# Performance work log

Hardware: AMD Instinct MI355X
Metric: run time of the kernel (lower is better)

Reference implementation:

```python
import jax, jax.numpy as jnp
import numpy as np

CE_W, DICE_W, BD_W = 1.0, 3.0, 2.0   # combined-loss lambdas
BPW = 10.0                            # boundary pixel weight
SMOOTH = 1e-6                         # dice smoothing
# cv2.getStructuringElement(cv2.MORPH_ELLIPSE, (5,5))
ELLIPSE5 = np.array([[0,0,1,0,0],
                     [1,1,1,1,1],
                     [1,1,1,1,1],
                     [1,1,1,1,1],
                     [0,0,1,0,0]], dtype=bool)


def setup_inputs() -> dict:
    key = jax.random.key(0)
    k1, k2 = jax.random.split(key)
    B, C, H, W = 8, 8, 512, 1024
    pred = jax.random.normal(k1, (B, C, H, W), dtype=jnp.float32)
    target = jax.random.randint(k2, (B, H, W), 0, C).astype(jnp.int32)
    return {"pred": pred, "target": target}


def _morph(mask, is_dilate):
    """Grayscale dilate/erode with 5x5 ellipse SE (matches cv2 default border:
    padding value never wins the max/min)."""
    pad_val = 0 if is_dilate else jnp.iinfo(jnp.int32).max
    p = jnp.pad(mask, ((0, 0), (2, 2), (2, 2)), constant_values=pad_val)
    H, W = mask.shape[1], mask.shape[2]
    out = None
    for dy in range(5):
        for dx in range(5):
            if not ELLIPSE5[dy, dx]:
                continue
            s = p[:, dy:dy + H, dx:dx + W]
            if out is None:
                out = s
            else:
                out = jnp.maximum(out, s) if is_dilate else jnp.minimum(out, s)
    return out


def reference(pred, target):
    B, C, H, W = pred.shape
    logp = jax.nn.log_softmax(pred, axis=1)                         # (B,C,H,W)
    # per-pixel cross entropy
    ce_map = -jnp.take_along_axis(logp, target[:, None], axis=1)[:, 0]  # (B,H,W)
    ce = ce_map.mean()
    # dice over softmax probs vs one-hot target
    probs = jnp.exp(logp)
    onehot = jax.nn.one_hot(target, C, dtype=pred.dtype, axis=1)    # (B,C,H,W)
    inter = jnp.sum(probs * onehot, axis=(2, 3))                    # (B,C)
    card = jnp.sum(probs, axis=(2, 3)) + jnp.sum(onehot, axis=(2, 3))
    dice = 1.0 - jnp.mean((2.0 * inter + SMOOTH) / (card + SMOOTH))
    # boundary mask = morphological gradient of the label map
    t = target.astype(jnp.int32)
    boundary = _morph(t, True) - _morph(t, False)                   # (B,H,W)
    wmap = jnp.where(boundary > 0, jnp.float32(BPW), jnp.float32(1.0))
    bd = jnp.mean(ce_map * wmap)
    return CE_W * ce + DICE_W * dice + BD_W * bd
```

## Files before the change

### kernel.cpp

```cpp
#include <hip/hip_runtime.h>
#include <math.h>

constexpr int B = 8, C = 8, H = 512, W = 1024;
constexpr int RH = 2;
constexpr int NT = 256;
constexpr float BPW = 10.0f;
constexpr float SMOOTH = 1e-6f;

constexpr int ACC_N = 2 * B + 3 * B * C;

constexpr int NVALS = 22;
constexpr int PSTRIDE = 24;

typedef float f32x4 __attribute__((ext_vector_type(4)));

__device__ __forceinline__ void gl_lds16(const float* g, float* l) {
    __builtin_amdgcn_global_load_lds(
        (const __attribute__((address_space(1))) void*)g,
        (__attribute__((address_space(3))) void*)l,
        16, 0, 0);
}

__device__ __forceinline__ unsigned win_or5(unsigned lo, unsigned mid, unsigned hi) {
    unsigned long long a = ((unsigned long long)mid << 32) | lo;
    unsigned long long b = ((unsigned long long)hi << 32) | mid;
    return (unsigned)(a >> 16) | (unsigned)(a >> 24) | mid |
           (unsigned)(b >> 8) | (unsigned)(b >> 16);
}

__device__ __forceinline__ unsigned pack_row(const int* __restrict__ tb, int gh, int gc) {
    if (gh < 0 || gh >= H || gc < 0 || gc >= W) return 0u;
    const int4 t4 = *reinterpret_cast<const int4*>(tb + (size_t)gh * W + gc);
    return (1u << t4.x) | ((1u << t4.y) << 8) | ((1u << t4.z) << 16) | ((1u << t4.w) << 24);
}

__global__ __launch_bounds__(NT)
void loss_main(const float* __restrict__ pred, const int* __restrict__ target,
               float* __restrict__ acc) {
    __shared__ float lds_pred[RH * C * W];
    __shared__ float sred[32 * PSTRIDE];

    const int tid = threadIdx.x;
    const int lane = tid & 63, wid = tid >> 6;
    const int h0 = blockIdx.x * RH;
    const int b  = blockIdx.y;
    const int gc = tid * 4;

    const int* tb = target + (size_t)b * H * W;
    const size_t plane = (size_t)H * W;

    const unsigned c0 = pack_row(tb, h0 - 2, gc);
    const unsigned c1 = pack_row(tb, h0 - 1, gc);
    const unsigned c2 = pack_row(tb, h0,     gc);
    const unsigned c3 = pack_row(tb, h0 + 1, gc);
    const unsigned c4 = pack_row(tb, h0 + 2, gc);
    const unsigned c5 = pack_row(tb, h0 + 3, gc);
    const unsigned l0 = pack_row(tb, h0 - 1, gc - 4);
    const unsigned l1 = pack_row(tb, h0,     gc - 4);
    const unsigned l2 = pack_row(tb, h0 + 1, gc - 4);
    const unsigned l3 = pack_row(tb, h0 + 2, gc - 4);
    const unsigned r0 = pack_row(tb, h0 - 1, gc + 4);
    const unsigned r1 = pack_row(tb, h0,     gc + 4);
    const unsigned r2 = pack_row(tb, h0 + 1, gc + 4);
    const unsigned r3 = pack_row(tb, h0 + 2, gc + 4);

    const int seg = wid * 256;
#pragma unroll
    for (int s = 0; s < RH; ++s)
#pragma unroll
        for (int c = 0; c < C; ++c) {
            const float* g = pred + ((size_t)(b * C + c)) * plane
                                  + (size_t)(h0 + s) * W + seg + lane * 4;
            float* l = &lds_pred[(s * C + c) * W + seg];
            gl_lds16(g, l);
        }

    const unsigned bmA = win_or5(l0 | l1 | l2, c1 | c2 | c3, r0 | r1 | r2) | c0 | c4;
    const unsigned bmB = win_or5(l1 | l2 | l3, c2 | c3 | c4, r1 | r2 | r3) | c1 | c5;

    __builtin_amdgcn_sched_barrier(0);
    asm volatile("s_waitcnt vmcnt(0)" ::: "memory");
    __builtin_amdgcn_sched_barrier(0);

    float ce_s = 0.f, bd_s = 0.f;
    float p_s[C], in_s[C];
    unsigned cnt = 0u;
#pragma unroll
    for (int c = 0; c < C; ++c) { p_s[c] = 0.f; in_s[c] = 0.f; }

#pragma unroll
    for (int s = 0; s < RH; ++s) {
        f32x4 x[C];
#pragma unroll
        for (int c = 0; c < C; ++c)
            x[c] = *reinterpret_cast<const f32x4*>(&lds_pred[(s * C + c) * W + gc]);

        const unsigned cmid = (s == 0) ? c2 : c3;
        const unsigned bm4  = (s == 0) ? bmA : bmB;

#pragma unroll
        for (int j = 0; j < 4; ++j) {
            const float x0 = (j==0)?x[0].x:(j==1)?x[0].y:(j==2)?x[0].z:x[0].w;
            const float x1 = (j==0)?x[1].x:(j==1)?x[1].y:(j==2)?x[1].z:x[1].w;
            const float x2 = (j==0)?x[2].x:(j==1)?x[2].y:(j==2)?x[2].z:x[2].w;
            const float x3 = (j==0)?x[3].x:(j==1)?x[3].y:(j==2)?x[3].z:x[3].w;
            const float x4 = (j==0)?x[4].x:(j==1)?x[4].y:(j==2)?x[4].z:x[4].w;
            const float x5 = (j==0)?x[5].x:(j==1)?x[5].y:(j==2)?x[5].z:x[5].w;
            const float x6 = (j==0)?x[6].x:(j==1)?x[6].y:(j==2)?x[6].z:x[6].w;
            const float x7 = (j==0)?x[7].x:(j==1)?x[7].y:(j==2)?x[7].z:x[7].w;

            const float e0 = __expf(x0), e1 = __expf(x1), e2 = __expf(x2), e3 = __expf(x3);
            const float e4 = __expf(x4), e5 = __expf(x5), e6 = __expf(x6), e7 = __expf(x7);
            const float sum = ((e0 + e1) + (e2 + e3)) + ((e4 + e5) + (e6 + e7));
            const float invs = __builtin_amdgcn_rcpf(sum);

            const unsigned cm  = (cmid >> (8 * j)) & 0xFFu;
            const unsigned bmj = (bm4  >> (8 * j)) & 0xFFu;
            const int t = 31 - __clz(cm);

            const float p0 = e0 * invs, p1 = e1 * invs, p2 = e2 * invs, p3 = e3 * invs;
            const float p4 = e4 * invs, p5 = e5 * invs, p6 = e6 * invs, p7 = e7 * invs;
            p_s[0] += p0; p_s[1] += p1; p_s[2] += p2; p_s[3] += p3;
            p_s[4] += p4; p_s[5] += p5; p_s[6] += p6; p_s[7] += p7;

            const bool b0 = (t == 0), b1 = (t == 1), b2 = (t == 2), b3 = (t == 3);
            const bool b4 = (t == 4), b5 = (t == 5), b6 = (t == 6), b7 = (t == 7);
            in_s[0] += b0 ? p0 : 0.f;  in_s[1] += b1 ? p1 : 0.f;
            in_s[2] += b2 ? p2 : 0.f;  in_s[3] += b3 ? p3 : 0.f;
            in_s[4] += b4 ? p4 : 0.f;  in_s[5] += b5 ? p5 : 0.f;
            in_s[6] += b6 ? p6 : 0.f;  in_s[7] += b7 ? p7 : 0.f;

            float pt = p0;
            pt = b1 ? p1 : pt;  pt = b2 ? p2 : pt;  pt = b3 ? p3 : pt;
            pt = b4 ? p4 : pt;  pt = b5 ? p5 : pt;  pt = b6 ? p6 : pt;
            pt = b7 ? p7 : pt;
            const float l = __logf(pt);
            const float wgt = (bmj & (bmj - 1u)) ? BPW : 1.f;
            ce_s -= l;
            bd_s = fmaf(-l, wgt, bd_s);
            cnt += 1u << (t << 2);
        }
    }

    float vals[NVALS];
    vals[0] = ce_s; vals[1] = bd_s;
#pragma unroll
    for (int c = 0; c < C; ++c) {
        vals[2 + c]  = p_s[c];
        vals[10 + c] = in_s[c];
    }
#pragma unroll
    for (int q = 0; q < 4; ++q) {
        const float lo = (float)((cnt >> (8 * q)) & 0xFu);
        const float hi = (float)((cnt >> (8 * q + 4)) & 0xFu);
        vals[18 + q] = lo + 4096.f * hi;
    }
#pragma unroll
    for (int k = 0; k < NVALS; ++k) {
        float v = vals[k];
        v += __shfl_down(v, 32, 64);
        v += __shfl_down(v, 16, 64);
        v += __shfl_down(v, 8, 64);
        vals[k] = v;
    }
    if (lane < 8) {
        const int p = wid * 8 + lane;
#pragma unroll
        for (int k = 0; k < NVALS; ++k) sred[p * PSTRIDE + k] = vals[k];
    }
    __syncthreads();

    const int k = tid >> 3, j = tid & 7;
    if (k < NVALS) {
        float v = sred[(0 * 8 + j) * PSTRIDE + k] + sred[(1 * 8 + j) * PSTRIDE + k]
                + sred[(2 * 8 + j) * PSTRIDE + k] + sred[(3 * 8 + j) * PSTRIDE + k];
        v += __shfl_down(v, 4, 64);
        v += __shfl_down(v, 2, 64);
        v += __shfl_down(v, 1, 64);
        if (j == 0) {
            if (k == 0)      atomicAdd(&acc[b], v);
            else if (k == 1) atomicAdd(&acc[B + b], v);
            else if (k < 10) atomicAdd(&acc[2 * B + b * C + (k - 2)], v);
            else if (k < 18) atomicAdd(&acc[2 * B + B * C + b * C + (k - 10)], v);
            else {
                const int q = k - 18;
                const float hi = floorf(v * (1.f / 4096.f));
                const float lo = v - 4096.f * hi;
                atomicAdd(&acc[2 * B + 2 * B * C + b * C + 2 * q],     lo);
                atomicAdd(&acc[2 * B + 2 * B * C + b * C + 2 * q + 1], hi);
            }
        }
    }
}

__global__ void loss_final(const float* __restrict__ acc, float* __restrict__ out) {
    const int i = threadIdx.x;
    const float psum  = acc[2 * B + i];
    const float inter = acc[2 * B + B * C + i];
    const float cnt   = acc[2 * B + 2 * B * C + i];
    float d = (2.f * inter + SMOOTH) / (psum + cnt + SMOOTH);
    float ce = (i < B) ? acc[i] : 0.f;
    float bd = (i < B) ? acc[B + i] : 0.f;
#pragma unroll
    for (int off = 32; off > 0; off >>= 1) d += __shfl_down(d, off, 64);
#pragma unroll
    for (int off = 4; off > 0; off >>= 1) {
        ce += __shfl_down(ce, off, 64);
        bd += __shfl_down(bd, off, 64);
    }
    if (i == 0) {
        const float N = (float)B * H * W;
        const float dice = 1.f - d / (float)(B * C);
        out[0] = 1.0f * (ce / N) + 3.0f * dice + 2.0f * (bd / N);
    }
}

extern "C" void kernel_launch(void* const* d_in, const int* in_sizes, int n_in,
                              void* d_out, int out_size, void* d_ws, size_t ws_size,
                              hipStream_t stream) {
    const float* pred = (const float*)d_in[0];
    const int* target = (const int*)d_in[1];
    float* acc = (float*)d_ws;
    float* out = (float*)d_out;

    hipMemsetAsync(acc, 0, ACC_N * sizeof(float), stream);

    dim3 grid(H / RH, B);
    loss_main<<<grid, NT, 0, stream>>>(pred, target, acc);
    loss_final<<<1, 64, 0, stream>>>(acc, out);
}
```

Measured before the change: 224.3 us.

## Process eight rows per block with double-buffered LDS prefetch and shared label halo

Each block now handles 8 rows instead of 2. It packs the label rows plus a halo into LDS once, so the boundary masks reuse neighbour data instead of re-reading target rows from global memory. Prediction rows are double-buffered in LDS with async global-to-LDS loads, so the next row's load overlaps compute on the current row. Per-class counts move to a 64-bit packed counter reduced as integers, which gives fewer atomics per pixel handled. In exchange the grid has four times fewer blocks and the LDS and register pressure is higher, which could lower occupancy.

```diff
diff --git a/kernel.cpp b/kernel.cpp
--- a/kernel.cpp
+++ b/kernel.cpp
@@ -2,7 +2,7 @@
 #include <math.h>
 
 constexpr int B = 8, C = 8, H = 512, W = 1024;
-constexpr int RH = 2;
+constexpr int ROWS = 8;
 constexpr int NT = 256;
 constexpr float BPW = 10.0f;
 constexpr float SMOOTH = 1e-6f;
@@ -10,7 +10,9 @@
 constexpr int ACC_N = 2 * B + 3 * B * C;
 
 constexpr int NVALS = 22;
-constexpr int PSTRIDE = 24;
+constexpr int PSTRIDE = 23;
+constexpr int TGROWS = ROWS + 4;
+constexpr int TSTRIDE = W / 4 + 2;
 
 typedef float f32x4 __attribute__((ext_vector_type(4)));
 
@@ -28,75 +30,102 @@
            (unsigned)(b >> 8) | (unsigned)(b >> 16);
 }
 
-__device__ __forceinline__ unsigned pack_row(const int* __restrict__ tb, int gh, int gc) {
-    if (gh < 0 || gh >= H || gc < 0 || gc >= W) return 0u;
-    const int4 t4 = *reinterpret_cast<const int4*>(tb + (size_t)gh * W + gc);
-    return (1u << t4.x) | ((1u << t4.y) << 8) | ((1u << t4.z) << 16) | ((1u << t4.w) << 24);
-}
-
 __global__ __launch_bounds__(NT)
 void loss_main(const float* __restrict__ pred, const int* __restrict__ target,
                float* __restrict__ acc) {
-    __shared__ float lds_pred[RH * C * W];
+    __shared__ float lds_pred[2 * C * W];
     __shared__ float sred[32 * PSTRIDE];
+    unsigned* tpk = reinterpret_cast<unsigned*>(&lds_pred[C * W]);
 
     const int tid = threadIdx.x;
     const int lane = tid & 63, wid = tid >> 6;
-    const int h0 = blockIdx.x * RH;
+    const int r0 = blockIdx.x * ROWS;
     const int b  = blockIdx.y;
     const int gc = tid * 4;
-
-    const int* tb = target + (size_t)b * H * W;
     const size_t plane = (size_t)H * W;
-
-    const unsigned c0 = pack_row(tb, h0 - 2, gc);
-    const unsigned c1 = pack_row(tb, h0 - 1, gc);
-    const unsigned c2 = pack_row(tb, h0,     gc);
-    const unsigned c3 = pack_row(tb, h0 + 1, gc);
-    const unsigned c4 = pack_row(tb, h0 + 2, gc);
-    const unsigned c5 = pack_row(tb, h0 + 3, gc);
-    const unsigned l0 = pack_row(tb, h0 - 1, gc - 4);
-    const unsigned l1 = pack_row(tb, h0,     gc - 4);
-    const unsigned l2 = pack_row(tb, h0 + 1, gc - 4);
-    const unsigned l3 = pack_row(tb, h0 + 2, gc - 4);
-    const unsigned r0 = pack_row(tb, h0 - 1, gc + 4);
-    const unsigned r1 = pack_row(tb, h0,     gc + 4);
-    const unsigned r2 = pack_row(tb, h0 + 1, gc + 4);
-    const unsigned r3 = pack_row(tb, h0 + 2, gc + 4);
-
+    const int* tb = target + (size_t)b * plane;
+    const float* pbase = pred + (size_t)b * C * plane;
     const int seg = wid * 256;
-#pragma unroll
-    for (int s = 0; s < RH; ++s)
-#pragma unroll
-        for (int c = 0; c < C; ++c) {
-            const float* g = pred + ((size_t)(b * C + c)) * plane
-                                  + (size_t)(h0 + s) * W + seg + lane * 4;
-            float* l = &lds_pred[(s * C + c) * W + seg];
-            gl_lds16(g, l);
-        }
-
-    const unsigned bmA = win_or5(l0 | l1 | l2, c1 | c2 | c3, r0 | r1 | r2) | c0 | c4;
-    const unsigned bmB = win_or5(l1 | l2 | l3, c2 | c3 | c4, r1 | r2 | r3) | c1 | c5;
-
+
+    int4 traw[TGROWS];
+#pragma unroll
+    for (int j = 0; j < TGROWS; ++j) {
+        int gh = r0 - 2 + j;
+        gh = gh < 0 ? 0 : (gh >= H ? H - 1 : gh);
+        traw[j] = *reinterpret_cast<const int4*>(tb + (size_t)gh * W + gc);
+    }
     __builtin_amdgcn_sched_barrier(0);
-    asm volatile("s_waitcnt vmcnt(0)" ::: "memory");
-    __builtin_amdgcn_sched_barrier(0);
+
+#pragma unroll
+    for (int c = 0; c < C; ++c)
+        gl_lds16(pbase + (size_t)c * plane + (size_t)r0 * W + seg + lane * 4,
+                 &lds_pred[c * W + seg]);
+
+#pragma unroll
+    for (int j = 0; j < TGROWS; ++j) {
+        const int gh = r0 - 2 + j;
+        const int4 t4 = traw[j];
+        const unsigned m = (1u << t4.x) | ((1u << t4.y) << 8) |
+                           ((1u << t4.z) << 16) | ((1u << t4.w) << 24);
+        tpk[j * TSTRIDE + 1 + tid] = (gh >= 0 && gh < H) ? m : 0u;
+    }
+    if (tid < 2 * TGROWS) {
+        const int j = tid >> 1;
+        tpk[j * TSTRIDE + ((tid & 1) ? (TSTRIDE - 1) : 0)] = 0u;
+    }
+    __syncthreads();
+
+    unsigned bm4s[ROWS], cmids[ROWS];
+    {
+        unsigned m[TGROWS], lf[TGROWS], rg[TGROWS];
+#pragma unroll
+        for (int j = 0; j < TGROWS; ++j) {
+            m[j]  = tpk[j * TSTRIDE + 1 + tid];
+            lf[j] = tpk[j * TSTRIDE + tid];
+            rg[j] = tpk[j * TSTRIDE + 2 + tid];
+        }
+#pragma unroll
+        for (int i = 0; i < ROWS; ++i) {
+            bm4s[i] = win_or5(lf[i+1] | lf[i+2] | lf[i+3],
+                              m[i+1]  | m[i+2]  | m[i+3],
+                              rg[i+1] | rg[i+2] | rg[i+3]) | m[i] | m[i+4];
+            cmids[i] = m[i + 2];
+        }
+    }
+    __syncthreads();
 
     float ce_s = 0.f, bd_s = 0.f;
     float p_s[C], in_s[C];
-    unsigned cnt = 0u;
+    unsigned long long cnt = 0ull;
 #pragma unroll
     for (int c = 0; c < C; ++c) { p_s[c] = 0.f; in_s[c] = 0.f; }
 
 #pragma unroll
-    for (int s = 0; s < RH; ++s) {
+    for (int i = 0; i < ROWS; ++i) {
+        const int cur = i & 1;
+        if (i < ROWS - 1) {
+            asm volatile("s_waitcnt lgkmcnt(0)" ::: "memory");
+            __builtin_amdgcn_sched_barrier(0);
+#pragma unroll
+            for (int c = 0; c < C; ++c)
+                gl_lds16(pbase + (size_t)c * plane + (size_t)(r0 + i + 1) * W + seg + lane * 4,
+                         &lds_pred[(cur ^ 1) * C * W + c * W + seg]);
+            __builtin_amdgcn_sched_barrier(0);
+            asm volatile("s_waitcnt vmcnt(8)" ::: "memory");
+            __builtin_amdgcn_sched_barrier(0);
+        } else {
+            __builtin_amdgcn_sched_barrier(0);
+            asm volatile("s_waitcnt vmcnt(0)" ::: "memory");
+            __builtin_amdgcn_sched_barrier(0);
+        }
+
+        const unsigned bm4  = bm4s[i];
+        const unsigned cmid = cmids[i];
+
         f32x4 x[C];
 #pragma unroll
         for (int c = 0; c < C; ++c)
-            x[c] = *reinterpret_cast<const f32x4*>(&lds_pred[(s * C + c) * W + gc]);
-
-        const unsigned cmid = (s == 0) ? c2 : c3;
-        const unsigned bm4  = (s == 0) ? bmA : bmB;
+            x[c] = *reinterpret_cast<const f32x4*>(&lds_pred[cur * C * W + c * W + gc]);
 
 #pragma unroll
         for (int j = 0; j < 4; ++j) {
@@ -138,11 +167,12 @@
             const float wgt = (bmj & (bmj - 1u)) ? BPW : 1.f;
             ce_s -= l;
             bd_s = fmaf(-l, wgt, bd_s);
-            cnt += 1u << (t << 2);
-        }
-    }
-
-    float vals[NVALS];
+            cnt += 1ull << (t << 3);
+        }
+    }
+
+    float vals[18];
+    unsigned uvals[4];
     vals[0] = ce_s; vals[1] = bd_s;
 #pragma unroll
     for (int c = 0; c < C; ++c) {
@@ -150,44 +180,60 @@
         vals[10 + c] = in_s[c];
     }
 #pragma unroll
-    for (int q = 0; q < 4; ++q) {
-        const float lo = (float)((cnt >> (8 * q)) & 0xFu);
-        const float hi = (float)((cnt >> (8 * q + 4)) & 0xFu);
-        vals[18 + q] = lo + 4096.f * hi;
-    }
-#pragma unroll
-    for (int k = 0; k < NVALS; ++k) {
+    for (int q = 0; q < 4; ++q)
+        uvals[q] = (unsigned)((cnt >> (16 * q)) & 0xFFull)
+                 | ((unsigned)((cnt >> (16 * q + 8)) & 0xFFull) << 16);
+
+#pragma unroll
+    for (int k = 0; k < 18; ++k) {
         float v = vals[k];
         v += __shfl_down(v, 32, 64);
         v += __shfl_down(v, 16, 64);
         v += __shfl_down(v, 8, 64);
         vals[k] = v;
     }
+#pragma unroll
+    for (int q = 0; q < 4; ++q) {
+        unsigned v = uvals[q];
+        v += (unsigned)__shfl_down((int)v, 32, 64);
+        v += (unsigned)__shfl_down((int)v, 16, 64);
+        v += (unsigned)__shfl_down((int)v, 8, 64);
+        uvals[q] = v;
+    }
+    unsigned* sredu = reinterpret_cast<unsigned*>(sred);
     if (lane < 8) {
         const int p = wid * 8 + lane;
 #pragma unroll
-        for (int k = 0; k < NVALS; ++k) sred[p * PSTRIDE + k] = vals[k];
+        for (int k = 0; k < 18; ++k) sred[p * PSTRIDE + k] = vals[k];
+#pragma unroll
+        for (int q = 0; q < 4; ++q) sredu[p * PSTRIDE + 18 + q] = uvals[q];
     }
     __syncthreads();
 
     const int k = tid >> 3, j = tid & 7;
     if (k < NVALS) {
-        float v = sred[(0 * 8 + j) * PSTRIDE + k] + sred[(1 * 8 + j) * PSTRIDE + k]
-                + sred[(2 * 8 + j) * PSTRIDE + k] + sred[(3 * 8 + j) * PSTRIDE + k];
-        v += __shfl_down(v, 4, 64);
-        v += __shfl_down(v, 2, 64);
-        v += __shfl_down(v, 1, 64);
-        if (j == 0) {
-            if (k == 0)      atomicAdd(&acc[b], v);
-            else if (k == 1) atomicAdd(&acc[B + b], v);
-            else if (k < 10) atomicAdd(&acc[2 * B + b * C + (k - 2)], v);
-            else if (k < 18) atomicAdd(&acc[2 * B + B * C + b * C + (k - 10)], v);
-            else {
-                const int q = k - 18;
-                const float hi = floorf(v * (1.f / 4096.f));
-                const float lo = v - 4096.f * hi;
-                atomicAdd(&acc[2 * B + 2 * B * C + b * C + 2 * q],     lo);
-                atomicAdd(&acc[2 * B + 2 * B * C + b * C + 2 * q + 1], hi);
+        if (k < 18) {
+            float v = sred[(0 * 8 + j) * PSTRIDE + k] + sred[(1 * 8 + j) * PSTRIDE + k]
+                    + sred[(2 * 8 + j) * PSTRIDE + k] + sred[(3 * 8 + j) * PSTRIDE + k];
+            v += __shfl_down(v, 4, 64);
+            v += __shfl_down(v, 2, 64);
+            v += __shfl_down(v, 1, 64);
+            if (j == 0) {
+                if (k == 0)      atomicAdd(&acc[b], v);
+                else if (k == 1) atomicAdd(&acc[B + b], v);
+                else if (k < 10) atomicAdd(&acc[2 * B + b * C + (k - 2)], v);
+                else             atomicAdd(&acc[2 * B + B * C + b * C + (k - 10)], v);
+            }
+        } else {
+            const int q = k - 18;
+            unsigned v = sredu[(0 * 8 + j) * PSTRIDE + k] + sredu[(1 * 8 + j) * PSTRIDE + k]
+                       + sredu[(2 * 8 + j) * PSTRIDE + k] + sredu[(3 * 8 + j) * PSTRIDE + k];
+            v += (unsigned)__shfl_down((int)v, 4, 64);
+            v += (unsigned)__shfl_down((int)v, 2, 64);
+            v += (unsigned)__shfl_down((int)v, 1, 64);
+            if (j == 0) {
+                atomicAdd(&acc[2 * B + 2 * B * C + b * C + 2 * q],     (float)(v & 0xFFFFu));
+                atomicAdd(&acc[2 * B + 2 * B * C + b * C + 2 * q + 1], (float)(v >> 16));
             }
         }
     }
@@ -225,7 +271,7 @@
 
     hipMemsetAsync(acc, 0, ACC_N * sizeof(float), stream);
 
-    dim3 grid(H / RH, B);
+    dim3 grid(H / ROWS, B);
     loss_main<<<grid, NT, 0, stream>>>(pred, target, acc);
     loss_final<<<1, 64, 0, stream>>>(acc, out);
 }
```

Result: faster. 210.5 us (median of 2 runs) (-6.1%).
